# Performance work log

Hardware: AMD Instinct MI355X
Metric: run time of the kernel (lower is better)

The kernel has to match this reference:

```python
import jax, jax.numpy as jnp
import numpy as np

D = 64          # node_hidden_dim
MP_STEPS = 6    # num_step_message_passing
S2S_STEPS = 6   # num_step_set2set
LSTM_LAYERS = 3 # num_layer_set2set


def setup_inputs() -> dict:
    key = jax.random.key(0)
    ks = jax.random.split(key, 32)
    N, E, B = 10000, 50000, 500
    node_in, edge_in, edge_hid, out_dim = 15, 5, 128, 12
    s = 0.1
    inp = {}
    inp["node_feat"] = jax.random.normal(ks[0], (N, node_in), jnp.float32)
    inp["edge_feat"] = jax.random.normal(ks[1], (E, edge_in), jnp.float32)
    inp["src"] = jax.random.randint(ks[2], (E,), 0, N)
    inp["dst"] = jax.random.randint(ks[3], (E,), 0, N)
    inp["graph_ids"] = jnp.sort(jax.random.randint(ks[4], (N,), 0, B))
    inp["num_graphs"] = B
    # lin0
    inp["lin0_W"] = jax.random.normal(ks[5], (node_in, D), jnp.float32) * s
    inp["lin0_b"] = jnp.zeros((D,), jnp.float32)
    # edge network MLP (Linear -> ReLU -> Linear), output reshaped to D x D per edge
    inp["em_W1"] = jax.random.normal(ks[6], (edge_in, edge_hid), jnp.float32) * s
    inp["em_b1"] = jnp.zeros((edge_hid,), jnp.float32)
    inp["em_W2"] = jax.random.normal(ks[7], (edge_hid, D * D), jnp.float32) * 0.02
    inp["em_b2"] = jnp.zeros((D * D,), jnp.float32)
    inp["conv_bias"] = jnp.zeros((D,), jnp.float32)
    # GRU (input D, hidden D), torch layout: [3*D, in], gate order r,z,n
    inp["gru_Wih"] = jax.random.normal(ks[8], (3 * D, D), jnp.float32) * s
    inp["gru_Whh"] = jax.random.normal(ks[9], (3 * D, D), jnp.float32) * s
    inp["gru_bih"] = jnp.zeros((3 * D,), jnp.float32)
    inp["gru_bhh"] = jnp.zeros((3 * D,), jnp.float32)
    # Set2Set LSTM: input 2*D, hidden D, 3 layers. torch layout [4*D, in], gates i,f,g,o
    inp["lstm0_Wih"] = jax.random.normal(ks[10], (4 * D, 2 * D), jnp.float32) * s
    inp["lstm0_Whh"] = jax.random.normal(ks[11], (4 * D, D), jnp.float32) * s
    inp["lstm0_bih"] = jnp.zeros((4 * D,), jnp.float32)
    inp["lstm0_bhh"] = jnp.zeros((4 * D,), jnp.float32)
    inp["lstm12_Wih"] = jax.random.normal(ks[12], (2, 4 * D, D), jnp.float32) * s
    inp["lstm12_Whh"] = jax.random.normal(ks[13], (2, 4 * D, D), jnp.float32) * s
    inp["lstm12_bih"] = jnp.zeros((2, 4 * D), jnp.float32)
    inp["lstm12_bhh"] = jnp.zeros((2, 4 * D), jnp.float32)
    # output head
    inp["lin1_W"] = jax.random.normal(ks[14], (2 * D, D), jnp.float32) * s
    inp["lin1_b"] = jnp.zeros((D,), jnp.float32)
    inp["lin2_W"] = jax.random.normal(ks[15], (D, out_dim), jnp.float32) * s
    inp["lin2_b"] = jnp.zeros((out_dim,), jnp.float32)
    return inp


def _mpnn(node_feat, edge_feat, src, dst, graph_ids, num_graphs,
          lin0_W, lin0_b, em_W1, em_b1, em_W2, em_b2, conv_bias,
          gru_Wih, gru_Whh, gru_bih, gru_bhh,
          lstm0_Wih, lstm0_Whh, lstm0_bih, lstm0_bhh,
          lstm12_Wih, lstm12_Whh, lstm12_bih, lstm12_bhh,
          lin1_W, lin1_b, lin2_W, lin2_b):
    N = node_feat.shape[0]
    E = edge_feat.shape[0]
    B = num_graphs
    # initial node embedding
    out = jax.nn.relu(node_feat @ lin0_W + lin0_b)      # [N, D]
    h = out                                             # GRU hidden (seq_len=1, 1 layer)
    # per-edge weight matrices (edge features are static across steps)
    We = (jax.nn.relu(edge_feat @ em_W1 + em_b1) @ em_W2 + em_b2).reshape(E, D, D)
    for _ in range(MP_STEPS):
        # NNConv: gather src -> per-edge matvec -> scatter-add to dst
        msg = jnp.einsum('ei,eio->eo', out[src], We)    # [E, D]
        agg = jax.ops.segment_sum(msg, dst, num_segments=N) + conv_bias
        m = jax.nn.relu(agg)                            # [N, D]
        # GRU cell (torch gate order r, z, n)
        gx = m @ gru_Wih.T + gru_bih
        gh = h @ gru_Whh.T + gru_bhh
        rx, zx, nx = jnp.split(gx, 3, axis=-1)
        rh, zh, nh = jnp.split(gh, 3, axis=-1)
        r = jax.nn.sigmoid(rx + rh)
        z = jax.nn.sigmoid(zx + zh)
        n = jnp.tanh(nx + r * nh)
        h = (1.0 - z) * n + z * h
        out = h
    # Set2Set readout: 3-layer LSTM over steps, attention over nodes per graph
    h_l = [jnp.zeros((B, D), out.dtype) for _ in range(LSTM_LAYERS)]
    c_l = [jnp.zeros((B, D), out.dtype) for _ in range(LSTM_LAYERS)]
    q_star = jnp.zeros((B, 2 * D), out.dtype)
    for _ in range(S2S_STEPS):
        x = q_star
        for l in range(LSTM_LAYERS):
            if l == 0:
                Wih, Whh, bih, bhh = lstm0_Wih, lstm0_Whh, lstm0_bih, lstm0_bhh
            else:
                Wih, Whh = lstm12_Wih[l - 1], lstm12_Whh[l - 1]
                bih, bhh = lstm12_bih[l - 1], lstm12_bhh[l - 1]
            g = x @ Wih.T + bih + h_l[l] @ Whh.T + bhh
            i_g, f_g, g_g, o_g = jnp.split(g, 4, axis=-1)
            c_l[l] = jax.nn.sigmoid(f_g) * c_l[l] + jax.nn.sigmoid(i_g) * jnp.tanh(g_g)
            h_l[l] = jax.nn.sigmoid(o_g) * jnp.tanh(c_l[l])
            x = h_l[l]
        q = x                                           # [B, D]
        # segment softmax attention
        e = jnp.sum(out * q[graph_ids], axis=-1)        # [N]
        emax = jax.ops.segment_max(e, graph_ids, num_segments=B)
        ex = jnp.exp(e - emax[graph_ids])
        denom = jax.ops.segment_sum(ex, graph_ids, num_segments=B)
        alpha = ex / denom[graph_ids]                   # [N]
        readout = jax.ops.segment_sum(alpha[:, None] * out, graph_ids, num_segments=B)
        q_star = jnp.concatenate([q, readout], axis=-1) # [B, 2D]
    y = jax.nn.relu(q_star @ lin1_W + lin1_b) @ lin2_W + lin2_b
    return y


def reference(node_feat, edge_feat, src, dst, graph_ids, num_graphs,
              lin0_W, lin0_b, em_W1, em_b1, em_W2, em_b2, conv_bias,
              gru_Wih, gru_Whh, gru_bih, gru_bhh,
              lstm0_Wih, lstm0_Whh, lstm0_bih, lstm0_bhh,
              lstm12_Wih, lstm12_Whh, lstm12_bih, lstm12_bhh,
              lin1_W, lin1_b, lin2_W, lin2_b):
    return _mpnn(node_feat, edge_feat, src, dst, graph_ids, num_graphs,
                 lin0_W, lin0_b, em_W1, em_b1, em_W2, em_b2, conv_bias,
                 gru_Wih, gru_Whh, gru_bih, gru_bhh,
                 lstm0_Wih, lstm0_Whh, lstm0_bih, lstm0_bhh,
                 lstm12_Wih, lstm12_Whh, lstm12_bih, lstm12_bhh,
                 lin1_W, lin1_b, lin2_W, lin2_b)
```

## Files before the change

### kernel.cpp

```cpp
#include <hip/hip_runtime.h>
#include <math.h>

#define NGRAPH 500
#define MP_STEPS 6
#define S2S_STEPS 6
#define S2S_CAP 64

typedef _Float16 h8 __attribute__((ext_vector_type(8)));
typedef float f4 __attribute__((ext_vector_type(4)));

__device__ __forceinline__ float sigmoidf_(float v){ return 1.0f/(1.0f + expf(-v)); }

__global__ void k_zero(float* __restrict__ p, int n){
  int i = blockIdx.x*256 + threadIdx.x;
  if(i < n) p[i] = 0.f;
}

__global__ void k_lin0(const float* __restrict__ nf, const float* __restrict__ W,
                       const float* __restrict__ b, const float* __restrict__ B2,
                       float* __restrict__ x, float* __restrict__ bm, int N){
  int n = blockIdx.x*4 + (threadIdx.x >> 6);
  int d = threadIdx.x & 63;
  if(n >= N) return;
  float acc = b[d];
#pragma unroll
  for(int i=0;i<15;i++) acc = fmaf(nf[n*15+i], W[i*64+d], acc);
  float xv = fmaxf(acc, 0.0f);
  x[n*64+d] = xv;
  float bmv = 0.f;
  for(int k=0;k<64;k++){
    float xk = __shfl(xv, k, 64);
    bmv = fmaf(xk, B2[k*64+d], bmv);
  }
  bm[(size_t)n*64+d] = bmv;
}

__global__ void k_edgeh(const float* __restrict__ ef, const float* __restrict__ W1,
                        const float* __restrict__ b1, _Float16* __restrict__ he, int E){
  int e = blockIdx.x*2 + (threadIdx.x >> 7);
  int h = threadIdx.x & 127;
  if(e >= E) return;
  float acc = b1[h];
#pragma unroll
  for(int i=0;i<5;i++) acc = fmaf(ef[e*5+i], W1[i*128+h], acc);
  he[(size_t)e*128 + h] = (_Float16)fmaxf(acc, 0.f);
}

__global__ void k_prepW2(const float* __restrict__ W2, _Float16* __restrict__ W2T){
  int idx = blockIdx.x*256 + threadIdx.x;
  if(idx >= 4096*128) return;
  int n = idx >> 7, k = idx & 127;
  W2T[idx] = (_Float16)W2[(size_t)k*4096 + n];
}

__global__ __launch_bounds__(256, 2) void k_fmsg(
    const _Float16* __restrict__ he,
    const _Float16* __restrict__ W2T,
    const float* __restrict__ x,
    const float* __restrict__ bm,
    const int* __restrict__ src, const int* __restrict__ dst,
    float* __restrict__ agg, int E)
{
  __shared__ _Float16 hs[128*128];
  __shared__ float xsT[64*132];
  __shared__ int ds_dst[128];
  __shared__ int ds_src[128];
  const int tid  = threadIdx.x;
  const int og   = tid >> 6;
  const int lane = tid & 63;
  const int quad = lane >> 4;
  const int l15  = lane & 15;
  const int e0   = blockIdx.x * 128;

  for(int t = tid; t < 2048; t += 256){
    int r = t >> 4, c = t & 15;
    uint4 v = make_uint4(0,0,0,0);
    if(e0 + r < E) v = *(const uint4*)&he[(size_t)(e0+r)*128 + c*8];
    *(uint4*)&hs[r*128 + c*8] = v;
  }
  {
    int j = tid >> 1, half = tid & 1;
    int sj = (e0 + j < E) ? src[e0 + j] : 0;
    const float4* xr = (const float4*)(x + (size_t)sj*64) + half*8;
#pragma unroll
    for(int k=0;k<8;k++){
      float4 v = xr[k];
      int ib = half*32 + k*4;
      xsT[(ib+0)*132 + j] = v.x;
      xsT[(ib+1)*132 + j] = v.y;
      xsT[(ib+2)*132 + j] = v.z;
      xsT[(ib+3)*132 + j] = v.w;
    }
  }
  if(tid < 128){
    ds_dst[tid] = (e0 + tid < E) ? dst[e0 + tid] : 0;
    ds_src[tid] = (e0 + tid < E) ? src[e0 + tid] : 0;
  }
  __syncthreads();

  h8 af[8][4];
#pragma unroll
  for(int mt=0;mt<8;mt++)
#pragma unroll
    for(int ks=0;ks<4;ks++)
      af[mt][ks] = *(const h8*)&hs[(mt*16 + l15)*128 + ks*32 + (quad<<3)];

  const _Float16* bbase = W2T + (size_t)(og*16 + l15)*128 + (quad<<3);

  f4 macc[8];
#pragma unroll
  for(int mt=0;mt<8;mt++) macc[mt] = (f4){0.f,0.f,0.f,0.f};

#pragma unroll 1
  for(int i=0;i<64;i++){
    const _Float16* bp = bbase + (size_t)i*64*128;
    h8 bf0 = *(const h8*)(bp);
    h8 bf1 = *(const h8*)(bp + 32);
    h8 bf2 = *(const h8*)(bp + 64);
    h8 bf3 = *(const h8*)(bp + 96);
    f4 g[8];
#pragma unroll
    for(int mt=0;mt<8;mt++) g[mt] = (f4){0.f,0.f,0.f,0.f};
#pragma unroll
    for(int mt=0;mt<8;mt++) g[mt] = __builtin_amdgcn_mfma_f32_16x16x32_f16(af[mt][0], bf0, g[mt], 0,0,0);
#pragma unroll
    for(int mt=0;mt<8;mt++) g[mt] = __builtin_amdgcn_mfma_f32_16x16x32_f16(af[mt][1], bf1, g[mt], 0,0,0);
#pragma unroll
    for(int mt=0;mt<8;mt++) g[mt] = __builtin_amdgcn_mfma_f32_16x16x32_f16(af[mt][2], bf2, g[mt], 0,0,0);
#pragma unroll
    for(int mt=0;mt<8;mt++) g[mt] = __builtin_amdgcn_mfma_f32_16x16x32_f16(af[mt][3], bf3, g[mt], 0,0,0);
#pragma unroll
    for(int mt=0;mt<8;mt++){
      f4 xf = *(const f4*)&xsT[i*132 + mt*16 + (quad<<2)];
      macc[mt] += xf * g[mt];
    }
  }

  const int col = og*16 + l15;
#pragma unroll
  for(int mt=0;mt<8;mt++){
#pragma unroll
    for(int r=0;r<4;r++){
      int edge = mt*16 + (quad<<2) + r;
      if(e0 + edge < E){
        float v = macc[mt][r] + bm[(size_t)ds_src[edge]*64 + col];
        atomicAdd(&agg[(size_t)ds_dst[edge]*64 + col], v);
      }
    }
  }
}

__global__ __launch_bounds__(256) void k_gru2(
    float* __restrict__ x, float* __restrict__ agg, const float* __restrict__ cb,
    const float* __restrict__ WihT, const float* __restrict__ WhhT,
    const float* __restrict__ bih, const float* __restrict__ bhh,
    const float* __restrict__ B2, float* __restrict__ bm, int N)
{
  __shared__ float ms[32*64], hs2[32*64];
  const int tid = threadIdx.x;
  const int n0 = blockIdx.x*32;
  for(int t=tid; t<2048; t+=256){
    int n = n0 + (t>>6), d = t&63;
    float mv=0.f, hv=0.f;
    if(n < N){
      mv = fmaxf(agg[(size_t)n*64+d] + cb[d], 0.f);
      agg[(size_t)n*64+d] = 0.f;
      hv = x[(size_t)n*64+d];
    }
    ms[t]=mv; hs2[t]=hv;
  }
  __syncthreads();
  const int gx = tid & 31, ng = tid >> 5;
  float ar[4][2]={{0}}, az[4][2]={{0}}, anx[4][2]={{0}}, anh[4][2]={{0}};
#pragma unroll 4
  for(int k=0;k<64;k++){
    float wi0=WihT[k*192+gx],     wi1=WihT[k*192+gx+32];
    float wi2=WihT[k*192+gx+64],  wi3=WihT[k*192+gx+96];
    float wi4=WihT[k*192+gx+128], wi5=WihT[k*192+gx+160];
    float wh0=WhhT[k*192+gx],     wh1=WhhT[k*192+gx+32];
    float wh2=WhhT[k*192+gx+64],  wh3=WhhT[k*192+gx+96];
    float wh4=WhhT[k*192+gx+128], wh5=WhhT[k*192+gx+160];
#pragma unroll
    for(int j=0;j<4;j++){
      float mk = ms[(ng*4+j)*64+k], hk = hs2[(ng*4+j)*64+k];
      ar[j][0] = fmaf(mk,wi0, fmaf(hk,wh0, ar[j][0]));
      ar[j][1] = fmaf(mk,wi1, fmaf(hk,wh1, ar[j][1]));
      az[j][0] = fmaf(mk,wi2, fmaf(hk,wh2, az[j][0]));
      az[j][1] = fmaf(mk,wi3, fmaf(hk,wh3, az[j][1]));
      anx[j][0]= fmaf(mk,wi4, anx[j][0]);
      anx[j][1]= fmaf(mk,wi5, anx[j][1]);
      anh[j][0]= fmaf(hk,wh4, anh[j][0]);
      anh[j][1]= fmaf(hk,wh5, anh[j][1]);
    }
  }
  float xn[4][2];
#pragma unroll
  for(int j=0;j<4;j++){
#pragma unroll
    for(int c=0;c<2;c++){
      int d = gx + 32*c;
      float r  = sigmoidf_(ar[j][c] + bih[d]     + bhh[d]);
      float z  = sigmoidf_(az[j][c] + bih[64+d]  + bhh[64+d]);
      float nn = tanhf(anx[j][c] + bih[128+d] + r*(anh[j][c] + bhh[128+d]));
      float hv = hs2[(ng*4+j)*64+d];
      xn[j][c] = (1.f - z)*nn + z*hv;
    }
  }
  __syncthreads();
#pragma unroll
  for(int j=0;j<4;j++){
#pragma unroll
    for(int c=0;c<2;c++){
      int n = n0 + ng*4 + j;
      ms[(ng*4+j)*64 + gx + 32*c] = xn[j][c];
      if(n < N) x[(size_t)n*64 + gx + 32*c] = xn[j][c];
    }
  }
  __syncthreads();
  float bmv[4][2] = {{0}};
#pragma unroll 4
  for(int d=0;d<64;d++){
    float b0 = B2[d*64+gx], b1 = B2[d*64+gx+32];
#pragma unroll
    for(int j=0;j<4;j++){
      float xd = ms[(ng*4+j)*64 + d];
      bmv[j][0] = fmaf(xd, b0, bmv[j][0]);
      bmv[j][1] = fmaf(xd, b1, bmv[j][1]);
    }
  }
#pragma unroll
  for(int j=0;j<4;j++){
    int n = n0 + ng*4 + j;
    if(n < N){
      bm[(size_t)n*64 + gx]      = bmv[j][0];
      bm[(size_t)n*64 + gx + 32] = bmv[j][1];
    }
  }
}

__global__ void k_tr_gru(const float* __restrict__ Wih, const float* __restrict__ Whh,
                         float* __restrict__ WihT, float* __restrict__ WhhT){
  int idx = blockIdx.x*256 + threadIdx.x;
  if(idx < 192*64){
    int r = idx/64, i = idx%64;
    WihT[i*192 + r] = Wih[idx];
    WhhT[i*192 + r] = Whh[idx];
  }
}

__global__ void k_tr_lstm(const float* __restrict__ w0ih, const float* __restrict__ w0hh,
                          const float* __restrict__ w12ih, const float* __restrict__ w12hh,
                          float* __restrict__ t0ih, float* __restrict__ t0hh,
                          float* __restrict__ t12ih, float* __restrict__ t12hh){
  int idx = blockIdx.x*256 + threadIdx.x;
  if(idx < 256*128){ int r = idx/128, k = idx%128; t0ih[k*256+r] = w0ih[idx]; }
  if(idx < 256*64){ int r = idx/64, k = idx%64; t0hh[k*256+r] = w0hh[idx]; }
  if(idx < 2*256*64){
    int l = idx/(256*64); int rem = idx%(256*64); int r = rem/64, k = rem%64;
    t12ih[l*64*256 + k*256 + r] = w12ih[idx];
    t12hh[l*64*256 + k*256 + r] = w12hh[idx];
  }
}

__device__ __forceinline__ int lbound(const int* __restrict__ a, int n, int v){
  int lo=0, hi=n;
  while(lo<hi){ int mid=(lo+hi)>>1; if(a[mid]<v) lo=mid+1; else hi=mid; }
  return lo;
}

template<int IN>
__device__ __forceinline__ void lstm_layer2(
    const float* __restrict__ xin, float* __restrict__ hv, float* __restrict__ cv,
    const float* __restrict__ WihT, const float* __restrict__ WhhT,
    const float* __restrict__ bi, const float* __restrict__ bh,
    float* __restrict__ gpart, int tid, int t, int hf)
{
  const int kx0 = hf*(IN/2);
  const int kh0 = hf*32;
  float a0=0.f,a1=0.f,a2=0.f,a3=0.f;
#pragma unroll
  for(int k=0;k<IN/2;k+=4){
    a0 = fmaf(xin[kx0+k+0], WihT[(kx0+k+0)*256+t], a0);
    a1 = fmaf(xin[kx0+k+1], WihT[(kx0+k+1)*256+t], a1);
    a2 = fmaf(xin[kx0+k+2], WihT[(kx0+k+2)*256+t], a2);
    a3 = fmaf(xin[kx0+k+3], WihT[(kx0+k+3)*256+t], a3);
  }
#pragma unroll
  for(int k=0;k<32;k+=4){
    a0 = fmaf(hv[kh0+k+0], WhhT[(kh0+k+0)*256+t], a0);
    a1 = fmaf(hv[kh0+k+1], WhhT[(kh0+k+1)*256+t], a1);
    a2 = fmaf(hv[kh0+k+2], WhhT[(kh0+k+2)*256+t], a2);
    a3 = fmaf(hv[kh0+k+3], WhhT[(kh0+k+3)*256+t], a3);
  }
  gpart[tid] = (a0+a1)+(a2+a3);
  __syncthreads();
  if(tid < 64){
    float gi = gpart[tid]     + gpart[256+tid] + bi[tid]     + bh[tid];
    float gf = gpart[64+tid]  + gpart[320+tid] + bi[64+tid]  + bh[64+tid];
    float gg = gpart[128+tid] + gpart[384+tid] + bi[128+tid] + bh[128+tid];
    float go = gpart[192+tid] + gpart[448+tid] + bi[192+tid] + bh[192+tid];
    float cn = sigmoidf_(gf)*cv[tid] + sigmoidf_(gi)*tanhf(gg);
    cv[tid] = cn;
    hv[tid] = sigmoidf_(go)*tanhf(cn);
  }
  __syncthreads();
}

__global__ __launch_bounds__(512) void k_s2s(
    const float* __restrict__ x, const int* __restrict__ gid, int N,
    const float* __restrict__ t0ih, const float* __restrict__ t0hh,
    const float* __restrict__ l0_bih, const float* __restrict__ l0_bhh,
    const float* __restrict__ t12ih, const float* __restrict__ t12hh,
    const float* __restrict__ l12_bih, const float* __restrict__ l12_bhh,
    const float* __restrict__ W1, const float* __restrict__ b1,
    const float* __restrict__ W2, const float* __restrict__ b2,
    float* __restrict__ y)
{
  const int b = blockIdx.x;
  const int tid = threadIdx.x;
  const int t = tid & 255, hf = tid >> 8;
  const int wave = tid >> 6, lane = tid & 63;
  __shared__ float xt[S2S_CAP*64];
  __shared__ float hsl[3][64], csl[3][64], qs[128], gpart[512];
  __shared__ float ps[S2S_CAP], rop[8*64], wred[8], wsum[8];
  __shared__ int sh_n0, sh_n1;

  if(tid == 0) sh_n0 = lbound(gid, N, b);
  if(tid == 1) sh_n1 = lbound(gid, N, b+1);
  if(tid < 192){ hsl[tid>>6][tid&63] = 0.f; csl[tid>>6][tid&63] = 0.f; }
  if(tid >= 192 && tid < 320) qs[tid-192] = 0.f;
  __syncthreads();
  const int n0 = sh_n0, cnt = sh_n1 - sh_n0;
  const int cc = (cnt < S2S_CAP) ? cnt : S2S_CAP;

  for(int j = wave; j < cc; j += 8)
    xt[j*64 + lane] = x[(size_t)(n0+j)*64 + lane];
  __syncthreads();

  for(int step=0; step<S2S_STEPS; step++){
    lstm_layer2<128>(qs,     hsl[0], csl[0], t0ih,           t0hh,           l0_bih,        l0_bhh,        gpart, tid, t, hf);
    lstm_layer2<64>(hsl[0],  hsl[1], csl[1], t12ih,          t12hh,          l12_bih,       l12_bhh,       gpart, tid, t, hf);
    lstm_layer2<64>(hsl[1],  hsl[2], csl[2], t12ih + 64*256, t12hh + 64*256, l12_bih + 256, l12_bhh + 256, gpart, tid, t, hf);

    float qv = hsl[2][lane];
    float pm = -1e30f;
    for(int j = wave; j < cc; j += 8){
      float p = xt[j*64 + lane] * qv;
#pragma unroll
      for(int o=32;o;o>>=1) p += __shfl_xor(p, o, 64);
      if(lane == 0) ps[j] = p;
      pm = fmaxf(pm, p);
    }
    for(int j = S2S_CAP + wave; j < cnt; j += 8){
      float p = x[(size_t)(n0+j)*64 + lane] * qv;
#pragma unroll
      for(int o=32;o;o>>=1) p += __shfl_xor(p, o, 64);
      pm = fmaxf(pm, p);
    }
    if(lane == 0) wred[wave] = pm;
    __syncthreads();
    float mx = wred[0];
#pragma unroll
    for(int w=1;w<8;w++) mx = fmaxf(mx, wred[w]);

    float pro = 0.f, pssum = 0.f;
    for(int j = wave; j < cc; j += 8){
      float ex = expf(ps[j] - mx);
      pssum += ex;
      pro = fmaf(ex, xt[j*64 + lane], pro);
    }
    for(int j = S2S_CAP + wave; j < cnt; j += 8){
      float xv = x[(size_t)(n0+j)*64 + lane];
      float p = xv * qv;
#pragma unroll
      for(int o=32;o;o>>=1) p += __shfl_xor(p, o, 64);
      float ex = expf(p - mx);
      pssum += ex;
      pro = fmaf(ex, xv, pro);
    }
    rop[wave*64 + lane] = pro;
    if(lane == 0) wsum[wave] = pssum;
    __syncthreads();
    if(tid < 64){
      float tot = 0.f;
#pragma unroll
      for(int w=0;w<8;w++) tot += wsum[w];
      float inv = (tot > 0.f) ? 1.f/tot : 0.f;
      float rv = 0.f;
#pragma unroll
      for(int w=0;w<8;w++) rv += rop[w*64+tid];
      qs[tid] = hsl[2][tid];
      qs[64+tid] = rv * inv;
    }
    __syncthreads();
  }
  if(tid < 64){
    float a = b1[tid];
#pragma unroll 4
    for(int k=0;k<128;k++) a = fmaf(qs[k], W1[k*64+tid], a);
    gpart[tid] = fmaxf(a, 0.f);
  }
  __syncthreads();
  if(tid < 12){
    float o = b2[tid];
#pragma unroll 4
    for(int k=0;k<64;k++) o = fmaf(gpart[k], W2[k*12+tid], o);
    y[b*12+tid] = o;
  }
}

extern "C" void kernel_launch(void* const* d_in, const int* in_sizes, int n_in,
                              void* d_out, int out_size, void* d_ws, size_t ws_size,
                              hipStream_t stream) {
  const float* node_feat = (const float*)d_in[0];
  const float* edge_feat = (const float*)d_in[1];
  const int*   src       = (const int*)d_in[2];
  const int*   dst       = (const int*)d_in[3];
  const int*   gid       = (const int*)d_in[4];
  const float* lin0_W = (const float*)d_in[6];
  const float* lin0_b = (const float*)d_in[7];
  const float* em_W1  = (const float*)d_in[8];
  const float* em_b1  = (const float*)d_in[9];
  const float* em_W2  = (const float*)d_in[10];
  const float* em_b2  = (const float*)d_in[11];
  const float* conv_b = (const float*)d_in[12];
  const float* gru_Wih = (const float*)d_in[13];
  const float* gru_Whh = (const float*)d_in[14];
  const float* gru_bih = (const float*)d_in[15];
  const float* gru_bhh = (const float*)d_in[16];
  const float* l0_Wih = (const float*)d_in[17];
  const float* l0_Whh = (const float*)d_in[18];
  const float* l0_bih = (const float*)d_in[19];
  const float* l0_bhh = (const float*)d_in[20];
  const float* l12_Wih = (const float*)d_in[21];
  const float* l12_Whh = (const float*)d_in[22];
  const float* l12_bih = (const float*)d_in[23];
  const float* l12_bhh = (const float*)d_in[24];
  const float* lin1_W = (const float*)d_in[25];
  const float* lin1_b = (const float*)d_in[26];
  const float* lin2_W = (const float*)d_in[27];
  const float* lin2_b = (const float*)d_in[28];
  float* y = (float*)d_out;

  const int N = in_sizes[0] / 15;
  const int E = in_sizes[1] / 5;
  const int B = NGRAPH;

  char* p = (char*)d_ws;
  auto carve = [&](size_t bytes)->char* {
    char* r = p; p += (bytes + 255) & ~(size_t)255; return r;
  };
  _Float16* he_h = (_Float16*)carve((size_t)E*128*2);
  _Float16* W2T  = (_Float16*)carve((size_t)4096*128*2);
  float* x     = (float*)carve((size_t)N*64*4);
  float* agg   = (float*)carve((size_t)N*64*4);
  float* bmv   = (float*)carve((size_t)N*64*4);
  float* gWihT = (float*)carve(192*64*4);
  float* gWhhT = (float*)carve(192*64*4);
  float* t0ih  = (float*)carve(128*256*4);
  float* t0hh  = (float*)carve(64*256*4);
  float* t12ih = (float*)carve(2*64*256*4);
  float* t12hh = (float*)carve(2*64*256*4);
  (void)ws_size; (void)n_in; (void)out_size;

  k_lin0<<<(N+3)/4, 256, 0, stream>>>(node_feat, lin0_W, lin0_b, em_b2, x, bmv, N);
  k_edgeh<<<(E+1)/2, 256, 0, stream>>>(edge_feat, em_W1, em_b1, he_h, E);
  k_prepW2<<<(4096*128+255)/256, 256, 0, stream>>>(em_W2, W2T);
  k_tr_gru<<<(192*64+255)/256, 256, 0, stream>>>(gru_Wih, gru_Whh, gWihT, gWhhT);
  k_tr_lstm<<<(2*256*64+255)/256, 256, 0, stream>>>(l0_Wih, l0_Whh, l12_Wih, l12_Whh,
                                                    t0ih, t0hh, t12ih, t12hh);
  k_zero<<<(N*64+255)/256, 256, 0, stream>>>(agg, N*64);

  const int nblk = (E + 127) / 128;
  for(int s=0; s<MP_STEPS; s++){
    k_fmsg<<<nblk, 256, 0, stream>>>(he_h, W2T, x, bmv, src, dst, agg, E);
    k_gru2<<<(N+31)/32, 256, 0, stream>>>(x, agg, conv_b, gWihT, gWhhT,
                                          gru_bih, gru_bhh, em_b2, bmv, N);
  }

  k_s2s<<<B, 512, 0, stream>>>(x, gid, N,
                               t0ih, t0hh, l0_bih, l0_bhh,
                               t12ih, t12hh, l12_bih, l12_bhh,
                               lin1_W, lin1_b, lin2_W, lin2_b, y);
}
```

Before: 962.8 us.

## Shrink edge tile with W2 prefetch and batch Set2Set over eight graphs per block

The fused message kernel now handles 64 edges per block instead of 128. This halves shared memory and the A-fragment register footprint, which should allow more resident blocks. It also software-prefetches the next W2T slice so the global load overlaps the MFMAs. The Set2Set kernel now processes 8 graphs per 256-thread block, so each LSTM weight load is reused across 8 graphs, and softmax attention reads x directly per wave. The trade-offs are reloading W2T twice as often overall and fewer, longer-running Set2Set blocks (63 blocks) with less parallelism.

```diff
diff --git a/kernel.cpp b/kernel.cpp
--- a/kernel.cpp
+++ b/kernel.cpp
@@ -4,7 +4,8 @@
 #define NGRAPH 500
 #define MP_STEPS 6
 #define S2S_STEPS 6
-#define S2S_CAP 64
+#define GPB 8
+#define PCAP 96
 
 typedef _Float16 h8 __attribute__((ext_vector_type(8)));
 typedef float f4 __attribute__((ext_vector_type(4)));
@@ -61,84 +62,88 @@
     const int* __restrict__ src, const int* __restrict__ dst,
     float* __restrict__ agg, int E)
 {
-  __shared__ _Float16 hs[128*128];
-  __shared__ float xsT[64*132];
-  __shared__ int ds_dst[128];
-  __shared__ int ds_src[128];
+  __shared__ _Float16 hs[64*128];
+  __shared__ float xsT[64*68];
+  __shared__ int ds_dst[64], ds_src[64];
   const int tid  = threadIdx.x;
   const int og   = tid >> 6;
   const int lane = tid & 63;
   const int quad = lane >> 4;
   const int l15  = lane & 15;
-  const int e0   = blockIdx.x * 128;
-
-  for(int t = tid; t < 2048; t += 256){
+  const int e0   = blockIdx.x * 64;
+
+  for(int t = tid; t < 1024; t += 256){
     int r = t >> 4, c = t & 15;
     uint4 v = make_uint4(0,0,0,0);
     if(e0 + r < E) v = *(const uint4*)&he[(size_t)(e0+r)*128 + c*8];
     *(uint4*)&hs[r*128 + c*8] = v;
   }
   {
-    int j = tid >> 1, half = tid & 1;
+    int j = tid >> 2, qc = tid & 3;
     int sj = (e0 + j < E) ? src[e0 + j] : 0;
-    const float4* xr = (const float4*)(x + (size_t)sj*64) + half*8;
-#pragma unroll
-    for(int k=0;k<8;k++){
-      float4 v = xr[k];
-      int ib = half*32 + k*4;
-      xsT[(ib+0)*132 + j] = v.x;
-      xsT[(ib+1)*132 + j] = v.y;
-      xsT[(ib+2)*132 + j] = v.z;
-      xsT[(ib+3)*132 + j] = v.w;
-    }
-  }
-  if(tid < 128){
+    const float4* xr = (const float4*)(x + (size_t)sj*64);
+#pragma unroll
+    for(int k=0;k<4;k++){
+      float4 v = xr[qc*4 + k];
+      int ib = qc*16 + k*4;
+      xsT[(ib+0)*68 + j] = v.x;
+      xsT[(ib+1)*68 + j] = v.y;
+      xsT[(ib+2)*68 + j] = v.z;
+      xsT[(ib+3)*68 + j] = v.w;
+    }
+  }
+  if(tid < 64){
     ds_dst[tid] = (e0 + tid < E) ? dst[e0 + tid] : 0;
     ds_src[tid] = (e0 + tid < E) ? src[e0 + tid] : 0;
   }
   __syncthreads();
 
-  h8 af[8][4];
-#pragma unroll
-  for(int mt=0;mt<8;mt++)
+  h8 af[4][4];
+#pragma unroll
+  for(int mt=0;mt<4;mt++)
 #pragma unroll
     for(int ks=0;ks<4;ks++)
       af[mt][ks] = *(const h8*)&hs[(mt*16 + l15)*128 + ks*32 + (quad<<3)];
 
   const _Float16* bbase = W2T + (size_t)(og*16 + l15)*128 + (quad<<3);
-
-  f4 macc[8];
-#pragma unroll
-  for(int mt=0;mt<8;mt++) macc[mt] = (f4){0.f,0.f,0.f,0.f};
-
-#pragma unroll 1
+  h8 bf[4], bn[4];
+#pragma unroll
+  for(int ks=0;ks<4;ks++) bf[ks] = *(const h8*)(bbase + ks*32);
+
+  f4 macc[4];
+#pragma unroll
+  for(int mt=0;mt<4;mt++) macc[mt] = (f4){0.f,0.f,0.f,0.f};
+
+#pragma unroll 2
   for(int i=0;i<64;i++){
-    const _Float16* bp = bbase + (size_t)i*64*128;
-    h8 bf0 = *(const h8*)(bp);
-    h8 bf1 = *(const h8*)(bp + 32);
-    h8 bf2 = *(const h8*)(bp + 64);
-    h8 bf3 = *(const h8*)(bp + 96);
-    f4 g[8];
-#pragma unroll
-    for(int mt=0;mt<8;mt++) g[mt] = (f4){0.f,0.f,0.f,0.f};
-#pragma unroll
-    for(int mt=0;mt<8;mt++) g[mt] = __builtin_amdgcn_mfma_f32_16x16x32_f16(af[mt][0], bf0, g[mt], 0,0,0);
-#pragma unroll
-    for(int mt=0;mt<8;mt++) g[mt] = __builtin_amdgcn_mfma_f32_16x16x32_f16(af[mt][1], bf1, g[mt], 0,0,0);
-#pragma unroll
-    for(int mt=0;mt<8;mt++) g[mt] = __builtin_amdgcn_mfma_f32_16x16x32_f16(af[mt][2], bf2, g[mt], 0,0,0);
-#pragma unroll
-    for(int mt=0;mt<8;mt++) g[mt] = __builtin_amdgcn_mfma_f32_16x16x32_f16(af[mt][3], bf3, g[mt], 0,0,0);
-#pragma unroll
-    for(int mt=0;mt<8;mt++){
-      f4 xf = *(const f4*)&xsT[i*132 + mt*16 + (quad<<2)];
-      macc[mt] += xf * g[mt];
-    }
+    if(i < 63){
+      const _Float16* nb = bbase + (size_t)(i+1)*64*128;
+#pragma unroll
+      for(int ks=0;ks<4;ks++) bn[ks] = *(const h8*)(nb + ks*32);
+    }
+    f4 g0 = (f4){0.f,0.f,0.f,0.f}, g1 = g0, g2 = g0, g3 = g0;
+#pragma unroll
+    for(int ks=0;ks<4;ks++){
+      g0 = __builtin_amdgcn_mfma_f32_16x16x32_f16(af[0][ks], bf[ks], g0, 0, 0, 0);
+      g1 = __builtin_amdgcn_mfma_f32_16x16x32_f16(af[1][ks], bf[ks], g1, 0, 0, 0);
+      g2 = __builtin_amdgcn_mfma_f32_16x16x32_f16(af[2][ks], bf[ks], g2, 0, 0, 0);
+      g3 = __builtin_amdgcn_mfma_f32_16x16x32_f16(af[3][ks], bf[ks], g3, 0, 0, 0);
+    }
+    f4 x0 = *(const f4*)&xsT[i*68 +  0 + (quad<<2)];
+    f4 x1 = *(const f4*)&xsT[i*68 + 16 + (quad<<2)];
+    f4 x2 = *(const f4*)&xsT[i*68 + 32 + (quad<<2)];
+    f4 x3 = *(const f4*)&xsT[i*68 + 48 + (quad<<2)];
+    macc[0] += x0 * g0;
+    macc[1] += x1 * g1;
+    macc[2] += x2 * g2;
+    macc[3] += x3 * g3;
+#pragma unroll
+    for(int ks=0;ks<4;ks++) bf[ks] = bn[ks];
   }
 
   const int col = og*16 + l15;
 #pragma unroll
-  for(int mt=0;mt<8;mt++){
+  for(int mt=0;mt<4;mt++){
 #pragma unroll
     for(int r=0;r<4;r++){
       int edge = mt*16 + (quad<<2) + r;
@@ -269,45 +274,65 @@
 }
 
 template<int IN>
-__device__ __forceinline__ void lstm_layer2(
-    const float* __restrict__ xin, float* __restrict__ hv, float* __restrict__ cv,
+__device__ __forceinline__ void lstm_g(
+    const float* __restrict__ xin,
+    float* __restrict__ hv,
+    float* __restrict__ cv,
     const float* __restrict__ WihT, const float* __restrict__ WhhT,
     const float* __restrict__ bi, const float* __restrict__ bh,
-    float* __restrict__ gpart, int tid, int t, int hf)
+    float (* __restrict__ gsg)[256], int tid)
 {
-  const int kx0 = hf*(IN/2);
-  const int kh0 = hf*32;
-  float a0=0.f,a1=0.f,a2=0.f,a3=0.f;
-#pragma unroll
-  for(int k=0;k<IN/2;k+=4){
-    a0 = fmaf(xin[kx0+k+0], WihT[(kx0+k+0)*256+t], a0);
-    a1 = fmaf(xin[kx0+k+1], WihT[(kx0+k+1)*256+t], a1);
-    a2 = fmaf(xin[kx0+k+2], WihT[(kx0+k+2)*256+t], a2);
-    a3 = fmaf(xin[kx0+k+3], WihT[(kx0+k+3)*256+t], a3);
-  }
-#pragma unroll
-  for(int k=0;k<32;k+=4){
-    a0 = fmaf(hv[kh0+k+0], WhhT[(kh0+k+0)*256+t], a0);
-    a1 = fmaf(hv[kh0+k+1], WhhT[(kh0+k+1)*256+t], a1);
-    a2 = fmaf(hv[kh0+k+2], WhhT[(kh0+k+2)*256+t], a2);
-    a3 = fmaf(hv[kh0+k+3], WhhT[(kh0+k+3)*256+t], a3);
-  }
-  gpart[tid] = (a0+a1)+(a2+a3);
-  __syncthreads();
-  if(tid < 64){
-    float gi = gpart[tid]     + gpart[256+tid] + bi[tid]     + bh[tid];
-    float gf = gpart[64+tid]  + gpart[320+tid] + bi[64+tid]  + bh[64+tid];
-    float gg = gpart[128+tid] + gpart[384+tid] + bi[128+tid] + bh[128+tid];
-    float go = gpart[192+tid] + gpart[448+tid] + bi[192+tid] + bh[192+tid];
-    float cn = sigmoidf_(gf)*cv[tid] + sigmoidf_(gi)*tanhf(gg);
-    cv[tid] = cn;
-    hv[tid] = sigmoidf_(go)*tanhf(cn);
-  }
-  __syncthreads();
-}
-
-__global__ __launch_bounds__(512) void k_s2s(
-    const float* __restrict__ x, const int* __restrict__ gid, int N,
+  float acc[GPB];
+#pragma unroll
+  for(int g=0;g<GPB;g++) acc[g]=0.f;
+#pragma unroll 2
+  for(int k=0;k<IN;k+=4){
+    float w0 = WihT[(k+0)*256+tid];
+    float w1 = WihT[(k+1)*256+tid];
+    float w2 = WihT[(k+2)*256+tid];
+    float w3 = WihT[(k+3)*256+tid];
+#pragma unroll
+    for(int g=0;g<GPB;g++){
+      f4 xv = *(const f4*)&xin[g*IN+k];
+      acc[g] = fmaf(xv[0], w0, acc[g]);
+      acc[g] = fmaf(xv[1], w1, acc[g]);
+      acc[g] = fmaf(xv[2], w2, acc[g]);
+      acc[g] = fmaf(xv[3], w3, acc[g]);
+    }
+  }
+#pragma unroll 2
+  for(int k=0;k<64;k+=4){
+    float w0 = WhhT[(k+0)*256+tid];
+    float w1 = WhhT[(k+1)*256+tid];
+    float w2 = WhhT[(k+2)*256+tid];
+    float w3 = WhhT[(k+3)*256+tid];
+#pragma unroll
+    for(int g=0;g<GPB;g++){
+      f4 hvv = *(const f4*)&hv[g*64+k];
+      acc[g] = fmaf(hvv[0], w0, acc[g]);
+      acc[g] = fmaf(hvv[1], w1, acc[g]);
+      acc[g] = fmaf(hvv[2], w2, acc[g]);
+      acc[g] = fmaf(hvv[3], w3, acc[g]);
+    }
+  }
+  float bb = bi[tid] + bh[tid];
+#pragma unroll
+  for(int g=0;g<GPB;g++) gsg[g][tid] = acc[g] + bb;
+  __syncthreads();
+#pragma unroll
+  for(int pp=0; pp<2; pp++){
+    int pair = tid + pp*256;
+    int g = pair >> 6, j = pair & 63;
+    float gi = gsg[g][j], gf = gsg[g][64+j], gg = gsg[g][128+j], go = gsg[g][192+j];
+    float cn = sigmoidf_(gf)*cv[g*64+j] + sigmoidf_(gi)*tanhf(gg);
+    cv[g*64+j] = cn;
+    hv[g*64+j] = sigmoidf_(go)*tanhf(cn);
+  }
+  __syncthreads();
+}
+
+__global__ __launch_bounds__(256) void k_s2s(
+    const float* __restrict__ x, const int* __restrict__ gid, int N, int B,
     const float* __restrict__ t0ih, const float* __restrict__ t0hh,
     const float* __restrict__ l0_bih, const float* __restrict__ l0_bhh,
     const float* __restrict__ t12ih, const float* __restrict__ t12hh,
@@ -316,96 +341,78 @@
     const float* __restrict__ W2, const float* __restrict__ b2,
     float* __restrict__ y)
 {
-  const int b = blockIdx.x;
-  const int tid = threadIdx.x;
-  const int t = tid & 255, hf = tid >> 8;
+  const int tid  = threadIdx.x;
   const int wave = tid >> 6, lane = tid & 63;
-  __shared__ float xt[S2S_CAP*64];
-  __shared__ float hsl[3][64], csl[3][64], qs[128], gpart[512];
-  __shared__ float ps[S2S_CAP], rop[8*64], wred[8], wsum[8];
-  __shared__ int sh_n0, sh_n1;
-
-  if(tid == 0) sh_n0 = lbound(gid, N, b);
-  if(tid == 1) sh_n1 = lbound(gid, N, b+1);
-  if(tid < 192){ hsl[tid>>6][tid&63] = 0.f; csl[tid>>6][tid&63] = 0.f; }
-  if(tid >= 192 && tid < 320) qs[tid-192] = 0.f;
-  __syncthreads();
-  const int n0 = sh_n0, cnt = sh_n1 - sh_n0;
-  const int cc = (cnt < S2S_CAP) ? cnt : S2S_CAP;
-
-  for(int j = wave; j < cc; j += 8)
-    xt[j*64 + lane] = x[(size_t)(n0+j)*64 + lane];
+  const int g0 = blockIdx.x * GPB;
+  __shared__ float hs3[3][GPB][64], cs3[3][GPB][64];
+  __shared__ float qsx[GPB][128];
+  __shared__ float gsg[GPB][256];
+  __shared__ float ps[GPB][PCAP];
+  __shared__ int ns[GPB+1];
+
+  if(tid <= GPB) ns[tid] = lbound(gid, N, g0 + tid);
+  for(int t=tid; t<3*GPB*64; t+=256){ (&hs3[0][0][0])[t]=0.f; (&cs3[0][0][0])[t]=0.f; }
+  for(int t=tid; t<GPB*128; t+=256) (&qsx[0][0])[t]=0.f;
   __syncthreads();
 
   for(int step=0; step<S2S_STEPS; step++){
-    lstm_layer2<128>(qs,     hsl[0], csl[0], t0ih,           t0hh,           l0_bih,        l0_bhh,        gpart, tid, t, hf);
-    lstm_layer2<64>(hsl[0],  hsl[1], csl[1], t12ih,          t12hh,          l12_bih,       l12_bhh,       gpart, tid, t, hf);
-    lstm_layer2<64>(hsl[1],  hsl[2], csl[2], t12ih + 64*256, t12hh + 64*256, l12_bih + 256, l12_bhh + 256, gpart, tid, t, hf);
-
-    float qv = hsl[2][lane];
-    float pm = -1e30f;
-    for(int j = wave; j < cc; j += 8){
-      float p = xt[j*64 + lane] * qv;
-#pragma unroll
-      for(int o=32;o;o>>=1) p += __shfl_xor(p, o, 64);
-      if(lane == 0) ps[j] = p;
-      pm = fmaxf(pm, p);
-    }
-    for(int j = S2S_CAP + wave; j < cnt; j += 8){
-      float p = x[(size_t)(n0+j)*64 + lane] * qv;
-#pragma unroll
-      for(int o=32;o;o>>=1) p += __shfl_xor(p, o, 64);
-      pm = fmaxf(pm, p);
-    }
-    if(lane == 0) wred[wave] = pm;
+    lstm_g<128>(&qsx[0][0],     &hs3[0][0][0], &cs3[0][0][0], t0ih,           t0hh,           l0_bih,        l0_bhh,        gsg, tid);
+    lstm_g<64>(&hs3[0][0][0],   &hs3[1][0][0], &cs3[1][0][0], t12ih,          t12hh,          l12_bih,       l12_bhh,       gsg, tid);
+    lstm_g<64>(&hs3[1][0][0],   &hs3[2][0][0], &cs3[2][0][0], t12ih + 64*256, t12hh + 64*256, l12_bih + 256, l12_bhh + 256, gsg, tid);
+
+    for(int gg = wave; gg < GPB; gg += 4){
+      int n0g = ns[gg], cntg = ns[gg+1] - ns[gg];
+      float qv = hs3[2][gg][lane];
+      float pm = -1e30f;
+      for(int j=0;j<cntg;j++){
+        float p = x[(size_t)(n0g+j)*64 + lane] * qv;
+#pragma unroll
+        for(int o=32;o;o>>=1) p += __shfl_xor(p, o, 64);
+        if(j < PCAP){ if(lane == 0) ps[gg][j] = p; }
+        pm = fmaxf(pm, p);
+      }
+      float pro = 0.f, pssum = 0.f;
+      for(int j=0;j<cntg;j++){
+        float xv = x[(size_t)(n0g+j)*64 + lane];
+        float p;
+        if(j < PCAP) p = ps[gg][j];
+        else {
+          p = xv * qv;
+#pragma unroll
+          for(int o=32;o;o>>=1) p += __shfl_xor(p, o, 64);
+        }
+        float ex = expf(p - pm);
+        pssum += ex;
+        pro = fmaf(ex, xv, pro);
+      }
+      float inv = (pssum > 0.f) ? 1.f/pssum : 0.f;
+      qsx[gg][lane]      = qv;
+      qsx[gg][64 + lane] = pro * inv;
+    }
     __syncthreads();
-    float mx = wred[0];
-#pragma unroll
-    for(int w=1;w<8;w++) mx = fmaxf(mx, wred[w]);
-
-    float pro = 0.f, pssum = 0.f;
-    for(int j = wave; j < cc; j += 8){
-      float ex = expf(ps[j] - mx);
-      pssum += ex;
-      pro = fmaf(ex, xt[j*64 + lane], pro);
-    }
-    for(int j = S2S_CAP + wave; j < cnt; j += 8){
-      float xv = x[(size_t)(n0+j)*64 + lane];
-      float p = xv * qv;
-#pragma unroll
-      for(int o=32;o;o>>=1) p += __shfl_xor(p, o, 64);
-      float ex = expf(p - mx);
-      pssum += ex;
-      pro = fmaf(ex, xv, pro);
-    }
-    rop[wave*64 + lane] = pro;
-    if(lane == 0) wsum[wave] = pssum;
-    __syncthreads();
-    if(tid < 64){
-      float tot = 0.f;
-#pragma unroll
-      for(int w=0;w<8;w++) tot += wsum[w];
-      float inv = (tot > 0.f) ? 1.f/tot : 0.f;
-      float rv = 0.f;
-#pragma unroll
-      for(int w=0;w<8;w++) rv += rop[w*64+tid];
-      qs[tid] = hsl[2][tid];
-      qs[64+tid] = rv * inv;
-    }
-    __syncthreads();
-  }
-  if(tid < 64){
-    float a = b1[tid];
+  }
+
+  {
+    int g = tid >> 6, j = tid & 63;
+#pragma unroll
+    for(int pp=0;pp<2;pp++){
+      int gg = g + pp*4;
+      float a = b1[j];
 #pragma unroll 4
-    for(int k=0;k<128;k++) a = fmaf(qs[k], W1[k*64+tid], a);
-    gpart[tid] = fmaxf(a, 0.f);
-  }
-  __syncthreads();
-  if(tid < 12){
-    float o = b2[tid];
+      for(int k=0;k<128;k++) a = fmaf(qsx[gg][k], W1[k*64+j], a);
+      gsg[gg][j] = fmaxf(a, 0.f);
+    }
+  }
+  __syncthreads();
+  if(tid < 96){
+    int gg = tid/12, oi = tid%12;
+    int gb = g0 + gg;
+    if(gb < B){
+      float o = b2[oi];
 #pragma unroll 4
-    for(int k=0;k<64;k++) o = fmaf(gpart[k], W2[k*12+tid], o);
-    y[b*12+tid] = o;
+      for(int k=0;k<64;k++) o = fmaf(gsg[gg][k], W2[k*12+oi], o);
+      y[gb*12+oi] = o;
+    }
   }
 }
 
@@ -471,14 +478,14 @@
                                                     t0ih, t0hh, t12ih, t12hh);
   k_zero<<<(N*64+255)/256, 256, 0, stream>>>(agg, N*64);
 
-  const int nblk = (E + 127) / 128;
+  const int nblk = (E + 63) / 64;
   for(int s=0; s<MP_STEPS; s++){
     k_fmsg<<<nblk, 256, 0, stream>>>(he_h, W2T, x, bmv, src, dst, agg, E);
     k_gru2<<<(N+31)/32, 256, 0, stream>>>(x, agg, conv_b, gWihT, gWhhT,
                                           gru_bih, gru_bhh, em_b2, bmv, N);
   }
 
-  k_s2s<<<B, 512, 0, stream>>>(x, gid, N,
+  k_s2s<<<(B+GPB-1)/GPB, 256, 0, stream>>>(x, gid, N, B,
                                t0ih, t0hh, l0_bih, l0_bhh,
                                t12ih, t12hh, l12_bih, l12_bhh,
                                lin1_W, lin1_b, lin2_W, lin2_b, y);
```

Result: slower. 1.498 ms (+55.6%).

## Drop LSTM weight transpose kernel; compute Set2Set gates per row with vector loads

Applied to the files above, without the earlier changes.

Removes the k_tr_lstm transpose launch and its workspace. The Set2Set kernel now reads the original row-major LSTM weights, with one thread per gate row doing the full dot product through float4 loads. The block shrinks from 512 to 256 threads, which drops the split-K partial-sum reduction. Each thread now reads its own 512-byte weight row, so neighbouring threads no longer make coalesced global reads. The LSTM dot products also become twice as long and serial per thread.

```diff
diff --git a/kernel.cpp b/kernel.cpp
--- a/kernel.cpp
+++ b/kernel.cpp
@@ -248,20 +248,6 @@
   }
 }
 
-__global__ void k_tr_lstm(const float* __restrict__ w0ih, const float* __restrict__ w0hh,
-                          const float* __restrict__ w12ih, const float* __restrict__ w12hh,
-                          float* __restrict__ t0ih, float* __restrict__ t0hh,
-                          float* __restrict__ t12ih, float* __restrict__ t12hh){
-  int idx = blockIdx.x*256 + threadIdx.x;
-  if(idx < 256*128){ int r = idx/128, k = idx%128; t0ih[k*256+r] = w0ih[idx]; }
-  if(idx < 256*64){ int r = idx/64, k = idx%64; t0hh[k*256+r] = w0hh[idx]; }
-  if(idx < 2*256*64){
-    int l = idx/(256*64); int rem = idx%(256*64); int r = rem/64, k = rem%64;
-    t12ih[l*64*256 + k*256 + r] = w12ih[idx];
-    t12hh[l*64*256 + k*256 + r] = w12hh[idx];
-  }
-}
-
 __device__ __forceinline__ int lbound(const int* __restrict__ a, int n, int v){
   int lo=0, hi=n;
   while(lo<hi){ int mid=(lo+hi)>>1; if(a[mid]<v) lo=mid+1; else hi=mid; }
@@ -269,89 +255,93 @@
 }
 
 template<int IN>
-__device__ __forceinline__ void lstm_layer2(
+__device__ __forceinline__ void lstm_row(
     const float* __restrict__ xin, float* __restrict__ hv, float* __restrict__ cv,
-    const float* __restrict__ WihT, const float* __restrict__ WhhT,
+    const float* __restrict__ Wih,
+    const float* __restrict__ Whh,
     const float* __restrict__ bi, const float* __restrict__ bh,
-    float* __restrict__ gpart, int tid, int t, int hf)
+    float* __restrict__ gs, int t)
 {
-  const int kx0 = hf*(IN/2);
-  const int kh0 = hf*32;
+  const float* wr = Wih + t*IN;
+  const float* hr = Whh + t*64;
   float a0=0.f,a1=0.f,a2=0.f,a3=0.f;
-#pragma unroll
-  for(int k=0;k<IN/2;k+=4){
-    a0 = fmaf(xin[kx0+k+0], WihT[(kx0+k+0)*256+t], a0);
-    a1 = fmaf(xin[kx0+k+1], WihT[(kx0+k+1)*256+t], a1);
-    a2 = fmaf(xin[kx0+k+2], WihT[(kx0+k+2)*256+t], a2);
-    a3 = fmaf(xin[kx0+k+3], WihT[(kx0+k+3)*256+t], a3);
-  }
-#pragma unroll
-  for(int k=0;k<32;k+=4){
-    a0 = fmaf(hv[kh0+k+0], WhhT[(kh0+k+0)*256+t], a0);
-    a1 = fmaf(hv[kh0+k+1], WhhT[(kh0+k+1)*256+t], a1);
-    a2 = fmaf(hv[kh0+k+2], WhhT[(kh0+k+2)*256+t], a2);
-    a3 = fmaf(hv[kh0+k+3], WhhT[(kh0+k+3)*256+t], a3);
-  }
-  gpart[tid] = (a0+a1)+(a2+a3);
-  __syncthreads();
-  if(tid < 64){
-    float gi = gpart[tid]     + gpart[256+tid] + bi[tid]     + bh[tid];
-    float gf = gpart[64+tid]  + gpart[320+tid] + bi[64+tid]  + bh[64+tid];
-    float gg = gpart[128+tid] + gpart[384+tid] + bi[128+tid] + bh[128+tid];
-    float go = gpart[192+tid] + gpart[448+tid] + bi[192+tid] + bh[192+tid];
-    float cn = sigmoidf_(gf)*cv[tid] + sigmoidf_(gi)*tanhf(gg);
-    cv[tid] = cn;
-    hv[tid] = sigmoidf_(go)*tanhf(cn);
-  }
-  __syncthreads();
-}
-
-__global__ __launch_bounds__(512) void k_s2s(
+#pragma unroll 8
+  for(int k=0;k<IN;k+=4){
+    f4 w = *(const f4*)&wr[k];
+    f4 xv = *(const f4*)&xin[k];
+    a0 = fmaf(w[0], xv[0], a0);
+    a1 = fmaf(w[1], xv[1], a1);
+    a2 = fmaf(w[2], xv[2], a2);
+    a3 = fmaf(w[3], xv[3], a3);
+  }
+#pragma unroll 8
+  for(int k=0;k<64;k+=4){
+    f4 w = *(const f4*)&hr[k];
+    f4 hvv = *(const f4*)&hv[k];
+    a0 = fmaf(w[0], hvv[0], a0);
+    a1 = fmaf(w[1], hvv[1], a1);
+    a2 = fmaf(w[2], hvv[2], a2);
+    a3 = fmaf(w[3], hvv[3], a3);
+  }
+  gs[t] = (a0+a1)+(a2+a3) + bi[t] + bh[t];
+  __syncthreads();
+  if(t < 64){
+    float ig = sigmoidf_(gs[t]);
+    float fg = sigmoidf_(gs[64+t]);
+    float gg = tanhf(gs[128+t]);
+    float og = sigmoidf_(gs[192+t]);
+    float cn = fg*cv[t] + ig*gg;
+    cv[t] = cn;
+    hv[t] = og*tanhf(cn);
+  }
+  __syncthreads();
+}
+
+__global__ __launch_bounds__(256) void k_s2s(
     const float* __restrict__ x, const int* __restrict__ gid, int N,
-    const float* __restrict__ t0ih, const float* __restrict__ t0hh,
+    const float* __restrict__ l0_Wih, const float* __restrict__ l0_Whh,
     const float* __restrict__ l0_bih, const float* __restrict__ l0_bhh,
-    const float* __restrict__ t12ih, const float* __restrict__ t12hh,
+    const float* __restrict__ l12_Wih, const float* __restrict__ l12_Whh,
     const float* __restrict__ l12_bih, const float* __restrict__ l12_bhh,
     const float* __restrict__ W1, const float* __restrict__ b1,
     const float* __restrict__ W2, const float* __restrict__ b2,
     float* __restrict__ y)
 {
   const int b = blockIdx.x;
-  const int tid = threadIdx.x;
-  const int t = tid & 255, hf = tid >> 8;
-  const int wave = tid >> 6, lane = tid & 63;
+  const int t = threadIdx.x;
+  const int wave = t >> 6, lane = t & 63;
   __shared__ float xt[S2S_CAP*64];
-  __shared__ float hsl[3][64], csl[3][64], qs[128], gpart[512];
-  __shared__ float ps[S2S_CAP], rop[8*64], wred[8], wsum[8];
+  __shared__ float hsl[3][64], csl[3][64], qs[128], gs[256];
+  __shared__ float ps[S2S_CAP], rop[4*64], wred[4], wsum[4];
   __shared__ int sh_n0, sh_n1;
 
-  if(tid == 0) sh_n0 = lbound(gid, N, b);
-  if(tid == 1) sh_n1 = lbound(gid, N, b+1);
-  if(tid < 192){ hsl[tid>>6][tid&63] = 0.f; csl[tid>>6][tid&63] = 0.f; }
-  if(tid >= 192 && tid < 320) qs[tid-192] = 0.f;
+  if(t == 0) sh_n0 = lbound(gid, N, b);
+  if(t == 1) sh_n1 = lbound(gid, N, b+1);
+  if(t < 192){ hsl[t>>6][t&63] = 0.f; csl[t>>6][t&63] = 0.f; }
+  if(t < 128) qs[t] = 0.f;
   __syncthreads();
   const int n0 = sh_n0, cnt = sh_n1 - sh_n0;
   const int cc = (cnt < S2S_CAP) ? cnt : S2S_CAP;
 
-  for(int j = wave; j < cc; j += 8)
+  for(int j = wave; j < cc; j += 4)
     xt[j*64 + lane] = x[(size_t)(n0+j)*64 + lane];
   __syncthreads();
 
   for(int step=0; step<S2S_STEPS; step++){
-    lstm_layer2<128>(qs,     hsl[0], csl[0], t0ih,           t0hh,           l0_bih,        l0_bhh,        gpart, tid, t, hf);
-    lstm_layer2<64>(hsl[0],  hsl[1], csl[1], t12ih,          t12hh,          l12_bih,       l12_bhh,       gpart, tid, t, hf);
-    lstm_layer2<64>(hsl[1],  hsl[2], csl[2], t12ih + 64*256, t12hh + 64*256, l12_bih + 256, l12_bhh + 256, gpart, tid, t, hf);
+    lstm_row<128>(qs,    hsl[0], csl[0], l0_Wih,            l0_Whh,            l0_bih,        l0_bhh,        gs, t);
+    lstm_row<64>(hsl[0], hsl[1], csl[1], l12_Wih,           l12_Whh,           l12_bih,       l12_bhh,       gs, t);
+    lstm_row<64>(hsl[1], hsl[2], csl[2], l12_Wih + 256*64,  l12_Whh + 256*64,  l12_bih + 256, l12_bhh + 256, gs, t);
 
     float qv = hsl[2][lane];
     float pm = -1e30f;
-    for(int j = wave; j < cc; j += 8){
+    for(int j = wave; j < cc; j += 4){
       float p = xt[j*64 + lane] * qv;
 #pragma unroll
       for(int o=32;o;o>>=1) p += __shfl_xor(p, o, 64);
       if(lane == 0) ps[j] = p;
       pm = fmaxf(pm, p);
     }
-    for(int j = S2S_CAP + wave; j < cnt; j += 8){
+    for(int j = S2S_CAP + wave; j < cnt; j += 4){
       float p = x[(size_t)(n0+j)*64 + lane] * qv;
 #pragma unroll
       for(int o=32;o;o>>=1) p += __shfl_xor(p, o, 64);
@@ -359,17 +349,15 @@
     }
     if(lane == 0) wred[wave] = pm;
     __syncthreads();
-    float mx = wred[0];
-#pragma unroll
-    for(int w=1;w<8;w++) mx = fmaxf(mx, wred[w]);
+    float mx = fmaxf(fmaxf(wred[0],wred[1]), fmaxf(wred[2],wred[3]));
 
     float pro = 0.f, pssum = 0.f;
-    for(int j = wave; j < cc; j += 8){
+    for(int j = wave; j < cc; j += 4){
       float ex = expf(ps[j] - mx);
       pssum += ex;
       pro = fmaf(ex, xt[j*64 + lane], pro);
     }
-    for(int j = S2S_CAP + wave; j < cnt; j += 8){
+    for(int j = S2S_CAP + wave; j < cnt; j += 4){
       float xv = x[(size_t)(n0+j)*64 + lane];
       float p = xv * qv;
 #pragma unroll
@@ -381,31 +369,27 @@
     rop[wave*64 + lane] = pro;
     if(lane == 0) wsum[wave] = pssum;
     __syncthreads();
-    if(tid < 64){
-      float tot = 0.f;
-#pragma unroll
-      for(int w=0;w<8;w++) tot += wsum[w];
+    if(t < 64){
+      float tot = wsum[0]+wsum[1]+wsum[2]+wsum[3];
       float inv = (tot > 0.f) ? 1.f/tot : 0.f;
-      float rv = 0.f;
-#pragma unroll
-      for(int w=0;w<8;w++) rv += rop[w*64+tid];
-      qs[tid] = hsl[2][tid];
-      qs[64+tid] = rv * inv;
+      float rv = (rop[t] + rop[64+t] + rop[128+t] + rop[192+t]) * inv;
+      qs[t] = hsl[2][t];
+      qs[64+t] = rv;
     }
     __syncthreads();
   }
-  if(tid < 64){
-    float a = b1[tid];
+  if(t < 64){
+    float a = b1[t];
 #pragma unroll 4
-    for(int k=0;k<128;k++) a = fmaf(qs[k], W1[k*64+tid], a);
-    gpart[tid] = fmaxf(a, 0.f);
-  }
-  __syncthreads();
-  if(tid < 12){
-    float o = b2[tid];
+    for(int k=0;k<128;k++) a = fmaf(qs[k], W1[k*64+t], a);
+    gs[t] = fmaxf(a, 0.f);
+  }
+  __syncthreads();
+  if(t < 12){
+    float o = b2[t];
 #pragma unroll 4
-    for(int k=0;k<64;k++) o = fmaf(gpart[k], W2[k*12+tid], o);
-    y[b*12+tid] = o;
+    for(int k=0;k<64;k++) o = fmaf(gs[k], W2[k*12+t], o);
+    y[b*12+t] = o;
   }
 }
 
@@ -457,18 +441,12 @@
   float* bmv   = (float*)carve((size_t)N*64*4);
   float* gWihT = (float*)carve(192*64*4);
   float* gWhhT = (float*)carve(192*64*4);
-  float* t0ih  = (float*)carve(128*256*4);
-  float* t0hh  = (float*)carve(64*256*4);
-  float* t12ih = (float*)carve(2*64*256*4);
-  float* t12hh = (float*)carve(2*64*256*4);
   (void)ws_size; (void)n_in; (void)out_size;
 
   k_lin0<<<(N+3)/4, 256, 0, stream>>>(node_feat, lin0_W, lin0_b, em_b2, x, bmv, N);
   k_edgeh<<<(E+1)/2, 256, 0, stream>>>(edge_feat, em_W1, em_b1, he_h, E);
   k_prepW2<<<(4096*128+255)/256, 256, 0, stream>>>(em_W2, W2T);
   k_tr_gru<<<(192*64+255)/256, 256, 0, stream>>>(gru_Wih, gru_Whh, gWihT, gWhhT);
-  k_tr_lstm<<<(2*256*64+255)/256, 256, 0, stream>>>(l0_Wih, l0_Whh, l12_Wih, l12_Whh,
-                                                    t0ih, t0hh, t12ih, t12hh);
   k_zero<<<(N*64+255)/256, 256, 0, stream>>>(agg, N*64);
 
   const int nblk = (E + 127) / 128;
@@ -478,8 +456,8 @@
                                           gru_bih, gru_bhh, em_b2, bmv, N);
   }
 
-  k_s2s<<<B, 512, 0, stream>>>(x, gid, N,
-                               t0ih, t0hh, l0_bih, l0_bhh,
-                               t12ih, t12hh, l12_bih, l12_bhh,
+  k_s2s<<<B, 256, 0, stream>>>(x, gid, N,
+                               l0_Wih, l0_Whh, l0_bih, l0_bhh,
+                               l12_Wih, l12_Whh, l12_bih, l12_bhh,
                                lin1_W, lin1_b, lin2_W, lin2_b, y);
 }
```

Result: no change. 978.3 us (+1.6%).
